# Kernel tuning notes

Measured on AMD Instinct MI355X. Metric: run time of the kernel, lower is better.

The kernel has to match this reference:

```python
import jax, jax.numpy as jnp
import numpy as np

BATCH = 8388608
D = 5

def setup_inputs() -> dict:
    key = jax.random.key(0)
    kx, kw, kb = jax.random.split(key, 3)
    x = jax.random.normal(kx, (BATCH, D), dtype=jnp.float32)
    W1 = jax.random.normal(kw, (D, D), dtype=jnp.float32) * 0.3
    b1 = jax.random.normal(kb, (D,), dtype=jnp.float32) * 0.1
    # fc2 chosen so the log() input stays positive (see shape_source):
    W2 = (-0.25) * jnp.eye(D, dtype=jnp.float32)
    b2 = 3.0 * jnp.ones((D,), dtype=jnp.float32)
    return {"x": x, "W1": W1, "b1": b1, "W2": W2, "b2": b2}

def reference(x, W1, b1, W2, b2):
    # preamble: ((x+1)*2 - 1) applied 3 times
    for _ in range(3):
        x = (x + 1.0) * 2.0 - 1.0
    for _ in range(3):
        x = jnp.cos(x)
        x = x @ W1.T + b1          # fc1
        x = jnp.sin(x)
        for _ in range(2):
            x = (x - 4.0) * 2.0
            x = x @ W2.T + b2      # fc2
            x = x - 4.0
        x = jnp.log(x)
        x = x @ W1.T + b1          # fc1
    return jnp.tanh(x * 6.0)
```

## Files before the change

kernel.cpp:

```cpp
#include <hip/hip_runtime.h>

#define TPB 256
#define RPT 4
#define D 5
#define F4PT 5
#define F4PB (TPB * F4PT)

__global__ __launch_bounds__(TPB, 4)
void uber_kernel(const float* __restrict__ x,
                 const float* __restrict__ W1,
                 const float* __restrict__ b1,
                 const float* __restrict__ W2,
                 const float* __restrict__ b2,
                 float* __restrict__ out)
{
    __shared__ float4 lds[F4PB];
    const int tid = threadIdx.x;
    const long long base4 = (long long)blockIdx.x * F4PB;

    const float4* __restrict__ src4 = reinterpret_cast<const float4*>(x) + base4;
    float4* __restrict__ dst4 = reinterpret_cast<float4*>(out) + base4;

    float4 stg[F4PT];
#pragma unroll
    for (int k = 0; k < F4PT; ++k) stg[k] = src4[k * TPB + tid];

    float w1[D][D], w2[D][D], bb1[D], bb2m4[D];
#pragma unroll
    for (int j = 0; j < D; ++j) {
        bb1[j] = b1[j];
        bb2m4[j] = b2[j] - 4.0f;
#pragma unroll
        for (int k = 0; k < D; ++k) {
            w1[j][k] = W1[j * D + k];
            w2[j][k] = W2[j * D + k];
        }
    }

#pragma unroll
    for (int k = 0; k < F4PT; ++k) lds[k * TPB + tid] = stg[k];
    __syncthreads();

    float f[RPT * D];
#pragma unroll
    for (int j = 0; j < F4PT; ++j) {
        float4 t = lds[F4PT * tid + j];
        f[4 * j + 0] = t.x; f[4 * j + 1] = t.y;
        f[4 * j + 2] = t.z; f[4 * j + 3] = t.w;
    }

#pragma unroll
    for (int r = 0; r < RPT; ++r) {
        float v[D];
#pragma unroll
        for (int c = 0; c < D; ++c) v[c] = fmaf(f[r * D + c], 8.0f, 7.0f);

#pragma unroll
        for (int it = 0; it < 3; ++it) {
            float t[D], u[D];
#pragma unroll
            for (int c = 0; c < D; ++c) t[c] = __cosf(v[c]);
#pragma unroll
            for (int j = 0; j < D; ++j) {
                float acc = bb1[j];
#pragma unroll
                for (int k = 0; k < D; ++k) acc = fmaf(t[k], w1[j][k], acc);
                u[j] = acc;
            }
#pragma unroll
            for (int c = 0; c < D; ++c) t[c] = __sinf(u[c]);
#pragma unroll
            for (int s = 0; s < 2; ++s) {
                float p[D];
#pragma unroll
                for (int c = 0; c < D; ++c) p[c] = fmaf(t[c], 2.0f, -8.0f);
#pragma unroll
                for (int j = 0; j < D; ++j) {
                    float acc = bb2m4[j];
#pragma unroll
                    for (int k = 0; k < D; ++k) acc = fmaf(p[k], w2[j][k], acc);
                    u[j] = acc;
                }
#pragma unroll
                for (int c = 0; c < D; ++c) t[c] = u[c];
            }
#pragma unroll
            for (int c = 0; c < D; ++c) t[c] = __logf(t[c]);
#pragma unroll
            for (int j = 0; j < D; ++j) {
                float acc = bb1[j];
#pragma unroll
                for (int k = 0; k < D; ++k) acc = fmaf(t[k], w1[j][k], acc);
                v[j] = acc;
            }
        }
#pragma unroll
        for (int c = 0; c < D; ++c) {
            float e = __expf(12.0f * v[c]);
            f[r * D + c] = 1.0f - __fdividef(2.0f, e + 1.0f);
        }
    }

#pragma unroll
    for (int j = 0; j < F4PT; ++j)
        lds[F4PT * tid + j] = make_float4(f[4 * j + 0], f[4 * j + 1],
                                          f[4 * j + 2], f[4 * j + 3]);
    __syncthreads();
#pragma unroll
    for (int k = 0; k < F4PT; ++k) dst4[k * TPB + tid] = lds[k * TPB + tid];
}

extern "C" void kernel_launch(void* const* d_in, const int* in_sizes, int n_in,
                              void* d_out, int out_size, void* d_ws, size_t ws_size,
                              hipStream_t stream) {
    const float* x  = (const float*)d_in[0];
    const float* W1 = (const float*)d_in[1];
    const float* b1 = (const float*)d_in[2];
    const float* W2 = (const float*)d_in[3];
    const float* b2 = (const float*)d_in[4];
    float* out = (float*)d_out;

    const int rows = in_sizes[0] / D;
    const int grid = rows / (TPB * RPT);
    uber_kernel<<<grid, TPB, 0, stream>>>(x, W1, b1, W2, b2, out);
}
```

Baseline: 356.1 us.

## Fold fc2 pair into one affine map and use native transcendental builtins

Precomputes algebraically folded constants in a small prep kernel: the two fc2 steps with their scale and shift become one 5x5 matrix plus bias, W1 and b1 are pre-scaled by 1/(2π) so the hardware sin/cos builtins can take revolutions directly, and the ln2 and exp-to-exp2 factors are folded in. The main kernel then calls the raw amdgcn sin, cos, log, exp2 and rcp intrinsics, removing one 5x5 matvec per iteration plus range-reduction and scaling work. The cost is an extra tiny kernel launch and possible accuracy changes from the folded constants and the raw intrinsics' limited input range. A fallback kernel computes the constants per thread when no workspace is available.

```diff
diff --git a/kernel.cpp b/kernel.cpp
--- a/kernel.cpp
+++ b/kernel.cpp
@@ -2,17 +2,140 @@
 
 #define TPB 256
 #define RPT 4
-#define D 5
+#define DD 5
 #define F4PT 5
 #define F4PB (TPB * F4PT)
 
-__global__ __launch_bounds__(TPB, 4)
-void uber_kernel(const float* __restrict__ x,
-                 const float* __restrict__ W1,
-                 const float* __restrict__ b1,
-                 const float* __restrict__ W2,
-                 const float* __restrict__ b2,
-                 float* __restrict__ out)
+#define INV2PI 0.15915494309189535f
+#define LN2f   0.6931471805599453f
+#define C2f    108.79849079439689f
+
+#define NCST 90
+
+__device__ __forceinline__ void compute_consts(const float* __restrict__ W1,
+                                               const float* __restrict__ b1,
+                                               const float* __restrict__ W2,
+                                               const float* __restrict__ b2,
+                                               float* cst)
+{
+#pragma unroll
+    for (int i = 0; i < 25; ++i) {
+        float w = W1[i];
+        cst[i]      = w * INV2PI;
+        cst[25 + i] = w * (LN2f * INV2PI);
+    }
+    float A[25], dv[DD];
+#pragma unroll
+    for (int j = 0; j < DD; ++j) {
+        float s = 0.0f;
+#pragma unroll
+        for (int k = 0; k < DD; ++k) {
+            float w = W2[j * DD + k];
+            A[j * DD + k] = 2.0f * w;
+            s += w;
+        }
+        dv[j] = b2[j] - 4.0f - 8.0f * s;
+    }
+#pragma unroll
+    for (int j = 0; j < DD; ++j)
+#pragma unroll
+        for (int k = 0; k < DD; ++k) {
+            float acc = 0.0f;
+#pragma unroll
+            for (int m = 0; m < DD; ++m) acc = fmaf(A[j * DD + m], A[m * DD + k], acc);
+            cst[50 + j * DD + k] = acc;
+        }
+#pragma unroll
+    for (int j = 0; j < DD; ++j) {
+        float acc = dv[j];
+#pragma unroll
+        for (int m = 0; m < DD; ++m) acc = fmaf(A[j * DD + m], dv[m], acc);
+        cst[75 + j] = acc;
+    }
+#pragma unroll
+    for (int j = 0; j < DD; ++j) {
+        cst[80 + j] = b1[j] * INV2PI;
+        cst[85 + j] = b1[j] * (12.0f / LN2f);
+    }
+}
+
+__global__ void prep_kernel(const float* __restrict__ W1, const float* __restrict__ b1,
+                            const float* __restrict__ W2, const float* __restrict__ b2,
+                            float* __restrict__ cst)
+{
+    if (threadIdx.x == 0 && blockIdx.x == 0) {
+        float c[NCST];
+        compute_consts(W1, b1, W2, b2, c);
+        for (int i = 0; i < NCST; ++i) cst[i] = c[i];
+    }
+}
+
+__device__ __forceinline__ void process_row(float* f,
+                                            const float* w1a, const float* w1b,
+                                            const float* m,   const float* ev,
+                                            const float* b1c, const float* b1t)
+{
+    float v[DD], t[DD], u[DD];
+#pragma unroll
+    for (int c = 0; c < DD; ++c) v[c] = fmaf(f[c], 8.0f * INV2PI, 7.0f * INV2PI);
+
+#pragma unroll
+    for (int it = 0; it < 3; ++it) {
+#pragma unroll
+        for (int c = 0; c < DD; ++c) t[c] = __builtin_amdgcn_cosf(v[c]);
+#pragma unroll
+        for (int j = 0; j < DD; ++j) {
+            float acc = b1c[j];
+#pragma unroll
+            for (int k = 0; k < DD; ++k) acc = fmaf(t[k], w1a[j * DD + k], acc);
+            u[j] = acc;
+        }
+#pragma unroll
+        for (int c = 0; c < DD; ++c) t[c] = __builtin_amdgcn_sinf(u[c]);
+#pragma unroll
+        for (int j = 0; j < DD; ++j) {
+            float acc = ev[j];
+#pragma unroll
+            for (int k = 0; k < DD; ++k) acc = fmaf(t[k], m[j * DD + k], acc);
+            u[j] = acc;
+        }
+#pragma unroll
+        for (int c = 0; c < DD; ++c) t[c] = __builtin_amdgcn_logf(u[c]);
+        if (it < 2) {
+#pragma unroll
+            for (int j = 0; j < DD; ++j) {
+                float acc = b1c[j];
+#pragma unroll
+                for (int k = 0; k < DD; ++k) acc = fmaf(t[k], w1b[j * DD + k], acc);
+                v[j] = acc;
+            }
+        } else {
+#pragma unroll
+            for (int c = 0; c < DD; ++c) t[c] *= C2f;
+#pragma unroll
+            for (int j = 0; j < DD; ++j) {
+                float acc = b1t[j];
+#pragma unroll
+                for (int k = 0; k < DD; ++k) acc = fmaf(t[k], w1b[j * DD + k], acc);
+                v[j] = acc;
+            }
+        }
+    }
+#pragma unroll
+    for (int c = 0; c < DD; ++c) {
+        float e2 = __builtin_amdgcn_exp2f(v[c]);
+        f[c] = fmaf(__builtin_amdgcn_rcpf(e2 + 1.0f), -2.0f, 1.0f);
+    }
+}
+
+template <bool LOCAL_CST>
+__device__ __forceinline__ void uber_body(const float* __restrict__ x,
+                                          const float* __restrict__ cstg,
+                                          const float* __restrict__ W1,
+                                          const float* __restrict__ b1,
+                                          const float* __restrict__ W2,
+                                          const float* __restrict__ b2,
+                                          float* __restrict__ out)
 {
     __shared__ float4 lds[F4PB];
     const int tid = threadIdx.x;
@@ -25,23 +148,25 @@
 #pragma unroll
     for (int k = 0; k < F4PT; ++k) stg[k] = src4[k * TPB + tid];
 
-    float w1[D][D], w2[D][D], bb1[D], bb2m4[D];
-#pragma unroll
-    for (int j = 0; j < D; ++j) {
-        bb1[j] = b1[j];
-        bb2m4[j] = b2[j] - 4.0f;
-#pragma unroll
-        for (int k = 0; k < D; ++k) {
-            w1[j][k] = W1[j * D + k];
-            w2[j][k] = W2[j * D + k];
-        }
-    }
+    float lc[LOCAL_CST ? NCST : 1];
+    const float* cst;
+    if (LOCAL_CST) {
+        compute_consts(W1, b1, W2, b2, lc);
+        cst = lc;
+    } else {
+        cst = cstg;
+    }
+    float w1a[25], w1b[25], m[25], ev[DD], b1c[DD], b1t[DD];
+#pragma unroll
+    for (int i = 0; i < 25; ++i) { w1a[i] = cst[i]; w1b[i] = cst[25 + i]; m[i] = cst[50 + i]; }
+#pragma unroll
+    for (int i = 0; i < DD; ++i) { ev[i] = cst[75 + i]; b1c[i] = cst[80 + i]; b1t[i] = cst[85 + i]; }
 
 #pragma unroll
     for (int k = 0; k < F4PT; ++k) lds[k * TPB + tid] = stg[k];
     __syncthreads();
 
-    float f[RPT * D];
+    float f[RPT * DD];
 #pragma unroll
     for (int j = 0; j < F4PT; ++j) {
         float4 t = lds[F4PT * tid + j];
@@ -50,56 +175,7 @@
     }
 
 #pragma unroll
-    for (int r = 0; r < RPT; ++r) {
-        float v[D];
-#pragma unroll
-        for (int c = 0; c < D; ++c) v[c] = fmaf(f[r * D + c], 8.0f, 7.0f);
-
-#pragma unroll
-        for (int it = 0; it < 3; ++it) {
-            float t[D], u[D];
-#pragma unroll
-            for (int c = 0; c < D; ++c) t[c] = __cosf(v[c]);
-#pragma unroll
-            for (int j = 0; j < D; ++j) {
-                float acc = bb1[j];
-#pragma unroll
-                for (int k = 0; k < D; ++k) acc = fmaf(t[k], w1[j][k], acc);
-                u[j] = acc;
-            }
-#pragma unroll
-            for (int c = 0; c < D; ++c) t[c] = __sinf(u[c]);
-#pragma unroll
-            for (int s = 0; s < 2; ++s) {
-                float p[D];
-#pragma unroll
-                for (int c = 0; c < D; ++c) p[c] = fmaf(t[c], 2.0f, -8.0f);
-#pragma unroll
-                for (int j = 0; j < D; ++j) {
-                    float acc = bb2m4[j];
-#pragma unroll
-                    for (int k = 0; k < D; ++k) acc = fmaf(p[k], w2[j][k], acc);
-                    u[j] = acc;
-                }
-#pragma unroll
-                for (int c = 0; c < D; ++c) t[c] = u[c];
-            }
-#pragma unroll
-            for (int c = 0; c < D; ++c) t[c] = __logf(t[c]);
-#pragma unroll
-            for (int j = 0; j < D; ++j) {
-                float acc = bb1[j];
-#pragma unroll
-                for (int k = 0; k < D; ++k) acc = fmaf(t[k], w1[j][k], acc);
-                v[j] = acc;
-            }
-        }
-#pragma unroll
-        for (int c = 0; c < D; ++c) {
-            float e = __expf(12.0f * v[c]);
-            f[r * D + c] = 1.0f - __fdividef(2.0f, e + 1.0f);
-        }
-    }
+    for (int r = 0; r < RPT; ++r) process_row(f + r * DD, w1a, w1b, m, ev, b1c, b1t);
 
 #pragma unroll
     for (int j = 0; j < F4PT; ++j)
@@ -108,6 +184,21 @@
     __syncthreads();
 #pragma unroll
     for (int k = 0; k < F4PT; ++k) dst4[k * TPB + tid] = lds[k * TPB + tid];
+}
+
+__global__ __launch_bounds__(TPB, 4)
+void uber_main(const float* __restrict__ x, const float* __restrict__ cst,
+               float* __restrict__ out)
+{
+    uber_body<false>(x, cst, nullptr, nullptr, nullptr, nullptr, out);
+}
+
+__global__ void uber_local(const float* __restrict__ x,
+                           const float* __restrict__ W1, const float* __restrict__ b1,
+                           const float* __restrict__ W2, const float* __restrict__ b2,
+                           float* __restrict__ out)
+{
+    uber_body<true>(x, nullptr, W1, b1, W2, b2, out);
 }
 
 extern "C" void kernel_launch(void* const* d_in, const int* in_sizes, int n_in,
@@ -120,7 +211,14 @@
     const float* b2 = (const float*)d_in[4];
     float* out = (float*)d_out;
 
-    const int rows = in_sizes[0] / D;
+    const int rows = in_sizes[0] / DD;
     const int grid = rows / (TPB * RPT);
-    uber_kernel<<<grid, TPB, 0, stream>>>(x, W1, b1, W2, b2, out);
-}
+
+    if (ws_size >= NCST * sizeof(float)) {
+        float* cst = (float*)d_ws;
+        prep_kernel<<<1, 64, 0, stream>>>(W1, b1, W2, b2, cst);
+        uber_main<<<grid, TPB, 0, stream>>>(x, cst, out);
+    } else {
+        uber_local<<<grid, TPB, 0, stream>>>(x, W1, b1, W2, b2, out);
+    }
+}
```

Result: faster. 292.1 us (-18.0%).
